# Performance work log

Hardware: AMD Instinct MI355X
Metric: run time of the kernel (lower is better)

## Reference

```python
import jax, jax.numpy as jnp
import numpy as np

N_NODES = 100000
MAX_CHILD = 8
X_SIZE = 128
H_SIZE = 128
N_TYPES = 8
W_SCALE = 0.05  # keep gates out of saturation


def setup_inputs() -> dict:
    key = jax.random.key(0)
    ks = jax.random.split(key, 8)
    return {
        "x": jax.random.normal(ks[0], (N_NODES, X_SIZE), jnp.float32),
        "n_h": jax.random.normal(ks[1], (N_NODES, MAX_CHILD, H_SIZE), jnp.float32),
        "n_c": jax.random.normal(ks[2], (N_NODES, MAX_CHILD, H_SIZE), jnp.float32),
        "type_id": jax.random.randint(ks[3], (N_NODES,), 0, N_TYPES, jnp.int64),
        "W_iou": jax.random.normal(ks[4], (N_TYPES, X_SIZE, 3 * H_SIZE), jnp.float32) * W_SCALE,
        "U_iou": jax.random.normal(ks[5], (N_TYPES, H_SIZE, 3 * H_SIZE), jnp.float32) * W_SCALE,
        "b_iou": jnp.zeros((N_TYPES, 3 * H_SIZE), jnp.float32),
        "U_f": jax.random.normal(ks[6], (N_TYPES, H_SIZE, H_SIZE), jnp.float32) * W_SCALE,
        "b_f": jnp.zeros((N_TYPES, H_SIZE), jnp.float32),
    }


def reference(x, n_h, n_c, type_id, W_iou, U_iou, b_iou, U_f, b_f):
    # x: [N, X], n_h/n_c: [N, K, H] child mailbox, type_id: [N]
    N, K, H = n_h.shape
    T = W_iou.shape[0]
    h_sum = n_h.sum(axis=1)  # child-sum is linear -> aggregate before GEMM [N, H]

    # --- reduce_func: masked per-type child aggregation ---
    iou_aggr = jnp.zeros((N, 3 * H), x.dtype)
    c_aggr = jnp.zeros((N, H), x.dtype)
    for t in range(T):
        m = (type_id == t)[:, None]
        iou_t = h_sum @ U_iou[t]                                   # [N, 3H]
        f = jax.nn.sigmoid(jnp.einsum("nkh,hg->nkg", n_h, U_f[t]) + b_f[t])
        c_t = (f * n_c).sum(axis=1)                                # [N, H]
        iou_aggr = jnp.where(m, iou_t, iou_aggr)
        c_aggr = jnp.where(m, c_t, c_aggr)

    # --- apply_node_func: masked per-type node states ---
    h_out = jnp.zeros((N, H), x.dtype)
    c_out = jnp.zeros((N, H), x.dtype)
    for t in range(T):
        m = (type_id == t)[:, None]
        iou = x @ W_iou[t] + iou_aggr + b_iou[t]                   # [N, 3H]
        i_g, o_g, u_g = jnp.split(iou, 3, axis=1)
        c_t = jax.nn.sigmoid(i_g) * jnp.tanh(u_g) + c_aggr
        h_t = jax.nn.sigmoid(o_g) * jnp.tanh(c_t)
        h_out = jnp.where(m, h_t, h_out)
        c_out = jnp.where(m, c_t, c_out)
    return h_out, c_out
```

## Files before the change

### kernel.cpp

```cpp
#include <hip/hip_runtime.h>
#include <hip/hip_bf16.h>
#include <stdint.h>

typedef __bf16 bf16x8 __attribute__((ext_vector_type(8)));
typedef float  f32x4  __attribute__((ext_vector_type(4)));

#define H    128
#define KCH  8
#define NT   8
#define BM   32

#define WS_TILET  2048
#define WS_IDX    16384
#define WS_UF     458752
#define WS_W      720896

__device__ __forceinline__ float fsigm(float v){ return 1.f/(1.f+__expf(-v)); }
__device__ __forceinline__ float ftanh(float v){
  v = fminf(fmaxf(v,-15.f),15.f);
  float e = __expf(2.f*v);
  return (e-1.f)/(e+1.f);
}

__global__ void k_init(int* ws){ if (threadIdx.x < 40) ws[threadIdx.x] = 0; }

__global__ void k_detect(const int* __restrict__ type_id, int* ws){
  __shared__ int nz;
  if (threadIdx.x == 0) nz = 0;
  __syncthreads();
  int v = type_id[threadIdx.x];
  if ((threadIdx.x & 1) && v != 0) atomicAdd(&nz, 1);
  __syncthreads();
  if (threadIdx.x == 0) ws[25] = (nz == 0) ? 2 : 1;
}

__global__ void k_count(const int* __restrict__ type_id, int* __restrict__ ws, int N){
  __shared__ int h[NT];
  int tid = threadIdx.x;
  if (tid < NT) h[tid] = 0;
  __syncthreads();
  int stride = ws[25];
  int i = blockIdx.x*blockDim.x + tid;
  if (i < N) atomicAdd(&h[type_id[(size_t)i*stride]], 1);
  __syncthreads();
  if (tid < NT) atomicAdd(&ws[tid], h[tid]);
}

__global__ void k_scan(int* m){
  int s = 0;
  for (int t=0;t<NT;++t){
    m[16+t] = s;
    m[8+t]  = s;
    m[26+t] = s + m[t];
    s += ((m[t]+BM-1)/BM)*BM;
  }
  m[24] = s;
}

__global__ void k_scatter(const int* __restrict__ type_id, int* __restrict__ ws, int N){
  __shared__ int h[NT], base[NT];
  int tid = threadIdx.x;
  if (tid < NT) h[tid] = 0;
  __syncthreads();
  int stride = ws[25];
  int i = blockIdx.x*blockDim.x + tid;
  int t = 0, lp = 0;
  if (i < N){ t = type_id[(size_t)i*stride]; lp = atomicAdd(&h[t], 1); }
  __syncthreads();
  if (tid < NT) base[tid] = atomicAdd(&ws[8+tid], h[tid]);
  __syncthreads();
  if (i < N) ws[(WS_IDX/4) + base[t] + lp] = i;
}

__global__ void k_tiletype(int* ws, int ntiles){
  int i = blockIdx.x*256 + threadIdx.x;
  if (i >= ntiles) return;
  const int* op = ws + 16;
  int p = i*BM, t = -1;
  if (p < op[8]){
    for (int s=0;s<NT;++s) if (p >= op[s] && p < op[s+1]) t = s;
  }
  ws[(WS_TILET/4) + i] = t;
}

__global__ void k_prep_uf(const float* __restrict__ U_f, char* __restrict__ ws){
  int gid = blockIdx.x*256 + threadIdx.x;
  if (gid >= NT*128*16) return;
  int sp = gid & 15, c = (gid>>4) & 127, t = gid >> 11;
  int kbase = 8*(sp ^ (c & 7));
  const float* src = U_f + ((size_t)t*H + kbase)*H + c;
  bf16x8 v;
  #pragma unroll
  for (int j=0;j<8;++j) v[j] = (__bf16)src[(size_t)j*H];
  *(bf16x8*)(ws + WS_UF + (size_t)gid*16) = v;
}

__global__ void k_prep_w(const float* __restrict__ W_iou, const float* __restrict__ U_iou,
                         char* __restrict__ ws){
  int gid = blockIdx.x*256 + threadIdx.x;
  if (gid >= NT*384*32) return;
  int sp = gid & 31, col = (gid>>5) % 384, t = gid / (384*32);
  int K0 = sp*8;
  bf16x8 v;
  #pragma unroll
  for (int j=0;j<8;++j){
    int K = K0 + j;
    float f = (K < H) ? W_iou[((size_t)t*H + K)*(3*H) + col]
                      : U_iou[((size_t)t*H + (K-H))*(3*H) + col];
    v[j] = (__bf16)f;
  }
  *(bf16x8*)(ws + WS_W + (size_t)gid*16) = v;
}

__global__ __launch_bounds__(256,4) void k_phaseB(
  const float* __restrict__ n_h, const float* __restrict__ n_c,
  const float* __restrict__ b_f, const char* __restrict__ ws,
  float* __restrict__ out, int N)
{
  __shared__ __align__(16) char lds[40960];
  const int* meta = (const int*)ws;
  int tile = blockIdx.x;
  int t = ((const int*)(ws + WS_TILET))[tile];
  if (t < 0) return;
  int ev = meta[26 + t];
  const int* idx = (const int*)(ws + WS_IDX);

  int tid = threadIdx.x;
  int lane = tid & 63, wave = tid >> 6;
  int rw = wave & 1, cw = wave >> 1;
  int l15 = lane & 15, l4 = lane >> 4;
  int base = tile*BM;

  int mrow = tid >> 3, mcol = (tid & 7) * 16;
  int mpos = base + mrow;
  int mnode = (mpos < ev) ? idx[mpos] : 0;

  int npos = base + rw*16 + l15;
  bool valn = npos < ev;
  int nd = valn ? idx[npos] : 0;
  const float* ncb = n_c + (size_t)nd*(KCH*H);
  int ocb[4]; f32x4 bf4[4];
  #pragma unroll
  for (int st=0; st<4; ++st){
    ocb[st] = cw*64 + st*16 + 4*l4;
    bf4[st] = *(const f32x4*)(b_f + t*H + ocb[st]);
  }

  {
    const char* src = ws + WS_UF + (size_t)t*32768;
    #pragma unroll
    for (int it=0; it<8; ++it){
      bf16x8 v = *(const bf16x8*)(src + it*4096 + tid*16);
      *(bf16x8*)(lds + it*4096 + tid*16) = v;
    }
  }

  const float* nh_base = n_h + (size_t)mnode*(KCH*H) + mcol;

  float hsum[16];
  #pragma unroll
  for (int j=0;j<16;++j) hsum[j] = 0.f;
  f32x4 cacc[4];
  #pragma unroll
  for (int st=0;st<4;++st) cacc[st] = (f32x4){0.f,0.f,0.f,0.f};

  int arow = rw*16 + l15;
  int aswz = (arow & 7) << 4;
  int mswz = (mrow & 7) << 4;

  for (int k=0;k<KCH;++k){
    {
      const float4* p = (const float4*)(nh_base + (size_t)k*H);
      float4 a0=p[0], a1=p[1], a2=p[2], a3=p[3];
      hsum[0]+=a0.x;  hsum[1]+=a0.y;  hsum[2]+=a0.z;  hsum[3]+=a0.w;
      hsum[4]+=a1.x;  hsum[5]+=a1.y;  hsum[6]+=a1.z;  hsum[7]+=a1.w;
      hsum[8]+=a2.x;  hsum[9]+=a2.y;  hsum[10]+=a2.z; hsum[11]+=a2.w;
      hsum[12]+=a3.x; hsum[13]+=a3.y; hsum[14]+=a3.z; hsum[15]+=a3.w;
      bf16x8 w0, w1;
      w0[0]=(__bf16)a0.x; w0[1]=(__bf16)a0.y; w0[2]=(__bf16)a0.z; w0[3]=(__bf16)a0.w;
      w0[4]=(__bf16)a1.x; w0[5]=(__bf16)a1.y; w0[6]=(__bf16)a1.z; w0[7]=(__bf16)a1.w;
      w1[0]=(__bf16)a2.x; w1[1]=(__bf16)a2.y; w1[2]=(__bf16)a2.z; w1[3]=(__bf16)a2.w;
      w1[4]=(__bf16)a3.x; w1[5]=(__bf16)a3.y; w1[6]=(__bf16)a3.z; w1[7]=(__bf16)a3.w;
      *(bf16x8*)(lds + 32768 + mrow*256 + (( mcol*2      ) ^ mswz)) = w0;
      *(bf16x8*)(lds + 32768 + mrow*256 + (( mcol*2 + 16 ) ^ mswz)) = w1;
    }
    __syncthreads();

    f32x4 fa[4];
    #pragma unroll
    for (int st=0;st<4;++st) fa[st] = (f32x4){0.f,0.f,0.f,0.f};
    #pragma unroll
    for (int kk=0; kk<4; ++kk){
      int kb = kk*64 + l4*16;
      bf16x8 bnh = *(const bf16x8*)(lds + 32768 + arow*256 + (kb ^ aswz));
      #pragma unroll
      for (int st=0;st<4;++st){
        int c = cw*64 + st*16 + l15;
        bf16x8 auf = *(const bf16x8*)(lds + c*256 + (kb ^ ((c&7)<<4)));
        fa[st] = __builtin_amdgcn_mfma_f32_16x16x32_bf16(auf, bnh, fa[st], 0,0,0);
      }
    }
    #pragma unroll
    for (int st=0;st<4;++st){
      f32x4 nc = *(const f32x4*)(ncb + k*H + ocb[st]);
      #pragma unroll
      for (int r=0;r<4;++r){
        float fg = fsigm(fa[st][r] + bf4[st][r]);
        cacc[st][r] += fg * nc[r];
      }
    }
    __syncthreads();
  }

  if (mpos < ev){
    float4* dst = (float4*)(out + (size_t)mnode*H + mcol);
    dst[0] = make_float4(hsum[0], hsum[1], hsum[2], hsum[3]);
    dst[1] = make_float4(hsum[4], hsum[5], hsum[6], hsum[7]);
    dst[2] = make_float4(hsum[8], hsum[9], hsum[10],hsum[11]);
    dst[3] = make_float4(hsum[12],hsum[13],hsum[14],hsum[15]);
  }
  float* outc = out + (size_t)N*H;
  if (valn){
    #pragma unroll
    for (int st=0;st<4;++st)
      *(f32x4*)(outc + (size_t)nd*H + ocb[st]) = cacc[st];
  }
}

__global__ __launch_bounds__(256,4) void k_phaseA(
  const float* __restrict__ x, const float* __restrict__ b_iou,
  const char* __restrict__ ws, float* __restrict__ out, int N)
{
  __shared__ __align__(16) char lds[16384];
  const int* meta = (const int*)ws;
  int tile = blockIdx.x;
  int t = ((const int*)(ws + WS_TILET))[tile];
  if (t < 0) return;
  int ev = meta[26 + t];
  const int* idx = (const int*)(ws + WS_IDX);

  int tid = threadIdx.x;
  int lane = tid & 63, wave = tid >> 6;
  int rw = wave & 1, cw = wave >> 1;
  int l15 = lane & 15, l4 = lane >> 4;
  int base = tile*BM;

  int mrow = tid >> 3, mcol = (tid & 7) * 16;
  int mpos = base + mrow;
  int mnode = (mpos < ev) ? idx[mpos] : 0;

  int npos = base + rw*16 + l15;
  bool valn = npos < ev;
  int nd = valn ? idx[npos] : 0;

  int mswz = (mrow & 7) << 4;
  {
    const float4* px = (const float4*)(x   + (size_t)mnode*H + mcol);
    const float4* ph = (const float4*)(out + (size_t)mnode*H + mcol);
    float4 x0=px[0], x1=px[1], x2=px[2], x3=px[3];
    float4 h0=ph[0], h1=ph[1], h2=ph[2], h3=ph[3];
    bf16x8 w0,w1,w2,w3;
    w0[0]=(__bf16)x0.x; w0[1]=(__bf16)x0.y; w0[2]=(__bf16)x0.z; w0[3]=(__bf16)x0.w;
    w0[4]=(__bf16)x1.x; w0[5]=(__bf16)x1.y; w0[6]=(__bf16)x1.z; w0[7]=(__bf16)x1.w;
    w1[0]=(__bf16)x2.x; w1[1]=(__bf16)x2.y; w1[2]=(__bf16)x2.z; w1[3]=(__bf16)x2.w;
    w1[4]=(__bf16)x3.x; w1[5]=(__bf16)x3.y; w1[6]=(__bf16)x3.z; w1[7]=(__bf16)x3.w;
    w2[0]=(__bf16)h0.x; w2[1]=(__bf16)h0.y; w2[2]=(__bf16)h0.z; w2[3]=(__bf16)h0.w;
    w2[4]=(__bf16)h1.x; w2[5]=(__bf16)h1.y; w2[6]=(__bf16)h1.z; w2[7]=(__bf16)h1.w;
    w3[0]=(__bf16)h2.x; w3[1]=(__bf16)h2.y; w3[2]=(__bf16)h2.z; w3[3]=(__bf16)h2.w;
    w3[4]=(__bf16)h3.x; w3[5]=(__bf16)h3.y; w3[6]=(__bf16)h3.z; w3[7]=(__bf16)h3.w;
    int ab = mrow*512;
    *(bf16x8*)(lds + ab + (( mcol*2            ) ^ mswz)) = w0;
    *(bf16x8*)(lds + ab + (( mcol*2 + 16       ) ^ mswz)) = w1;
    *(bf16x8*)(lds + ab + (( 256 + mcol*2      ) ^ mswz)) = w2;
    *(bf16x8*)(lds + ab + (( 256 + mcol*2 + 16 ) ^ mswz)) = w3;
  }
  __syncthreads();

  int arow = rw*16 + l15;
  int aswz = (arow & 7) << 4;
  float* outc = out + (size_t)N*H;
  const char* wbase = ws + WS_W + (size_t)t*(384*256*2);

  #pragma unroll
  for (int st=0; st<4; ++st){
    int ocb = cw*64 + st*16 + 4*l4;
    f32x4 ag[3];
    #pragma unroll
    for (int g=0;g<3;++g) ag[g] = (f32x4){0.f,0.f,0.f,0.f};
    const char* wrow = wbase + (size_t)(cw*64 + st*16 + l15)*512;
    #pragma unroll 1
    for (int kc=0;kc<4;++kc){
      #pragma unroll
      for (int kk2=0;kk2<2;++kk2){
        int kb = kc*128 + kk2*64 + l4*16;
        bf16x8 bact = *(const bf16x8*)(lds + arow*512 + (kb ^ aswz));
        #pragma unroll
        for (int g=0;g<3;++g){
          bf16x8 aW = *(const bf16x8*)(wrow + (size_t)(g*128)*512 + kb);
          ag[g] = __builtin_amdgcn_mfma_f32_16x16x32_bf16(aW, bact, ag[g], 0,0,0);
        }
      }
    }
    if (valn){
      f32x4 bi4 = *(const f32x4*)(b_iou + t*(3*H) +        ocb);
      f32x4 bo4 = *(const f32x4*)(b_iou + t*(3*H) + H   +  ocb);
      f32x4 bu4 = *(const f32x4*)(b_iou + t*(3*H) + 2*H +  ocb);
      f32x4 ca  = *(const f32x4*)(outc + (size_t)nd*H + ocb);
      f32x4 hv4, cv4;
      #pragma unroll
      for (int r=0;r<4;++r){
        float ig = ag[0][r] + bi4[r];
        float og = ag[1][r] + bo4[r];
        float ug = ag[2][r] + bu4[r];
        float cv = fsigm(ig)*ftanh(ug) + ca[r];
        float hv = fsigm(og)*ftanh(cv);
        cv4[r] = cv; hv4[r] = hv;
      }
      *(f32x4*)(out  + (size_t)nd*H + ocb) = hv4;
      *(f32x4*)(outc + (size_t)nd*H + ocb) = cv4;
    }
  }
}

extern "C" void kernel_launch(void* const* d_in, const int* in_sizes, int n_in,
                              void* d_out, int out_size, void* d_ws, size_t ws_size,
                              hipStream_t stream){
  const float* x      = (const float*)d_in[0];
  const float* n_h    = (const float*)d_in[1];
  const float* n_c    = (const float*)d_in[2];
  const int*   typ    = (const int*)d_in[3];
  const float* W_iou  = (const float*)d_in[4];
  const float* U_iou  = (const float*)d_in[5];
  const float* b_iou  = (const float*)d_in[6];
  const float* U_f    = (const float*)d_in[7];
  const float* b_f    = (const float*)d_in[8];
  float* out = (float*)d_out;
  int*   ws  = (int*)d_ws;
  char*  wsc = (char*)d_ws;
  int N = in_sizes[0] / H;
  int nb = (N + 255) / 256;
  int ntiles = (N + NT*(BM-1) + BM-1) / BM;

  hipLaunchKernelGGL(k_init,     dim3(1),   dim3(64),  0, stream, ws);
  hipLaunchKernelGGL(k_detect,   dim3(1),   dim3(256), 0, stream, typ, ws);
  hipLaunchKernelGGL(k_count,    dim3(nb),  dim3(256), 0, stream, typ, ws, N);
  hipLaunchKernelGGL(k_scan,     dim3(1),   dim3(1),   0, stream, ws);
  hipLaunchKernelGGL(k_scatter,  dim3(nb),  dim3(256), 0, stream, typ, ws, N);
  hipLaunchKernelGGL(k_tiletype, dim3((ntiles+255)/256), dim3(256), 0, stream, ws, ntiles);
  hipLaunchKernelGGL(k_prep_uf,  dim3((NT*128*16+255)/256), dim3(256), 0, stream, U_f, wsc);
  hipLaunchKernelGGL(k_prep_w,   dim3((NT*384*32+255)/256), dim3(256), 0, stream, W_iou, U_iou, wsc);
  hipLaunchKernelGGL(k_phaseB,   dim3(ntiles), dim3(256), 0, stream,
                     n_h, n_c, b_f, wsc, out, N);
  hipLaunchKernelGGL(k_phaseA,   dim3(ntiles), dim3(256), 0, stream,
                     x, b_iou, wsc, out, N);
}
```

Baseline: 428.9 us.

## Load child hidden states straight into MFMA operands, dropping LDS staging and barriers

In phase B, each lane now reads its n_h fragment directly from global memory into registers in the layout the MFMA B operand expects. This replaces the earlier cooperative load into an LDS buffer, which needed two __syncthreads per child iteration. The child-sum h is also accumulated from these registers, with each column-wave writing its half of the output, and the LDS footprint shrinks to hold only the U_f tile. In exchange, both column-waves load the same n_h rows, doubling global or L2 read traffic for n_h. The child loop is also no longer unrolled.

```diff
diff --git a/kernel.cpp b/kernel.cpp
--- a/kernel.cpp
+++ b/kernel.cpp
@@ -117,7 +117,7 @@
   const float* __restrict__ b_f, const char* __restrict__ ws,
   float* __restrict__ out, int N)
 {
-  __shared__ __align__(16) char lds[40960];
+  __shared__ __align__(16) char lds[32768];
   const int* meta = (const int*)ws;
   int tile = blockIdx.x;
   int t = ((const int*)(ws + WS_TILET))[tile];
@@ -131,13 +131,10 @@
   int l15 = lane & 15, l4 = lane >> 4;
   int base = tile*BM;
 
-  int mrow = tid >> 3, mcol = (tid & 7) * 16;
-  int mpos = base + mrow;
-  int mnode = (mpos < ev) ? idx[mpos] : 0;
-
   int npos = base + rw*16 + l15;
   bool valn = npos < ev;
   int nd = valn ? idx[npos] : 0;
+  const float* nhb = n_h + (size_t)nd*(KCH*H);
   const float* ncb = n_c + (size_t)nd*(KCH*H);
   int ocb[4]; f32x4 bf4[4];
   #pragma unroll
@@ -154,76 +151,71 @@
       *(bf16x8*)(lds + it*4096 + tid*16) = v;
     }
   }
-
-  const float* nh_base = n_h + (size_t)mnode*(KCH*H) + mcol;
-
-  float hsum[16];
-  #pragma unroll
-  for (int j=0;j<16;++j) hsum[j] = 0.f;
+  __syncthreads();
+
   f32x4 cacc[4];
   #pragma unroll
   for (int st=0;st<4;++st) cacc[st] = (f32x4){0.f,0.f,0.f,0.f};
-
-  int arow = rw*16 + l15;
-  int aswz = (arow & 7) << 4;
-  int mswz = (mrow & 7) << 4;
-
+  f32x4 hsv0 = {0,0,0,0}, hsv1 = {0,0,0,0}, hsv2 = {0,0,0,0}, hsv3 = {0,0,0,0};
+
+  #pragma unroll 1
   for (int k=0;k<KCH;++k){
-    {
-      const float4* p = (const float4*)(nh_base + (size_t)k*H);
-      float4 a0=p[0], a1=p[1], a2=p[2], a3=p[3];
-      hsum[0]+=a0.x;  hsum[1]+=a0.y;  hsum[2]+=a0.z;  hsum[3]+=a0.w;
-      hsum[4]+=a1.x;  hsum[5]+=a1.y;  hsum[6]+=a1.z;  hsum[7]+=a1.w;
-      hsum[8]+=a2.x;  hsum[9]+=a2.y;  hsum[10]+=a2.z; hsum[11]+=a2.w;
-      hsum[12]+=a3.x; hsum[13]+=a3.y; hsum[14]+=a3.z; hsum[15]+=a3.w;
-      bf16x8 w0, w1;
-      w0[0]=(__bf16)a0.x; w0[1]=(__bf16)a0.y; w0[2]=(__bf16)a0.z; w0[3]=(__bf16)a0.w;
-      w0[4]=(__bf16)a1.x; w0[5]=(__bf16)a1.y; w0[6]=(__bf16)a1.z; w0[7]=(__bf16)a1.w;
-      w1[0]=(__bf16)a2.x; w1[1]=(__bf16)a2.y; w1[2]=(__bf16)a2.z; w1[3]=(__bf16)a2.w;
-      w1[4]=(__bf16)a3.x; w1[5]=(__bf16)a3.y; w1[6]=(__bf16)a3.z; w1[7]=(__bf16)a3.w;
-      *(bf16x8*)(lds + 32768 + mrow*256 + (( mcol*2      ) ^ mswz)) = w0;
-      *(bf16x8*)(lds + 32768 + mrow*256 + (( mcol*2 + 16 ) ^ mswz)) = w1;
-    }
-    __syncthreads();
+    const float* rowp = nhb + (size_t)k*H + l4*8;
+    f32x4 L0 = *(const f32x4*)(rowp +  0);
+    f32x4 L1 = *(const f32x4*)(rowp +  4);
+    f32x4 L2 = *(const f32x4*)(rowp + 32);
+    f32x4 L3 = *(const f32x4*)(rowp + 36);
+    f32x4 L4 = *(const f32x4*)(rowp + 64);
+    f32x4 L5 = *(const f32x4*)(rowp + 68);
+    f32x4 L6 = *(const f32x4*)(rowp + 96);
+    f32x4 L7 = *(const f32x4*)(rowp +100);
+
+    if (cw == 0){ hsv0 += L0; hsv1 += L1; hsv2 += L2; hsv3 += L3; }
+    else        { hsv0 += L4; hsv1 += L5; hsv2 += L6; hsv3 += L7; }
+
+    bf16x8 bn0, bn1, bn2, bn3;
+    #pragma unroll
+    for (int j=0;j<4;++j){
+      bn0[j]=(__bf16)L0[j]; bn0[4+j]=(__bf16)L1[j];
+      bn1[j]=(__bf16)L2[j]; bn1[4+j]=(__bf16)L3[j];
+      bn2[j]=(__bf16)L4[j]; bn2[4+j]=(__bf16)L5[j];
+      bn3[j]=(__bf16)L6[j]; bn3[4+j]=(__bf16)L7[j];
+    }
 
     f32x4 fa[4];
     #pragma unroll
     for (int st=0;st<4;++st) fa[st] = (f32x4){0.f,0.f,0.f,0.f};
     #pragma unroll
-    for (int kk=0; kk<4; ++kk){
-      int kb = kk*64 + l4*16;
-      bf16x8 bnh = *(const bf16x8*)(lds + 32768 + arow*256 + (kb ^ aswz));
-      #pragma unroll
-      for (int st=0;st<4;++st){
-        int c = cw*64 + st*16 + l15;
-        bf16x8 auf = *(const bf16x8*)(lds + c*256 + (kb ^ ((c&7)<<4)));
-        fa[st] = __builtin_amdgcn_mfma_f32_16x16x32_bf16(auf, bnh, fa[st], 0,0,0);
-      }
-    }
-    #pragma unroll
     for (int st=0;st<4;++st){
-      f32x4 nc = *(const f32x4*)(ncb + k*H + ocb[st]);
+      int c = cw*64 + st*16 + l15;
+      int cs = (c&7)<<4;
+      const char* crow = lds + c*256;
+      fa[st] = __builtin_amdgcn_mfma_f32_16x16x32_bf16(*(const bf16x8*)(crow + ((  0 + l4*16) ^ cs)), bn0, fa[st], 0,0,0);
+      fa[st] = __builtin_amdgcn_mfma_f32_16x16x32_bf16(*(const bf16x8*)(crow + (( 64 + l4*16) ^ cs)), bn1, fa[st], 0,0,0);
+      fa[st] = __builtin_amdgcn_mfma_f32_16x16x32_bf16(*(const bf16x8*)(crow + ((128 + l4*16) ^ cs)), bn2, fa[st], 0,0,0);
+      fa[st] = __builtin_amdgcn_mfma_f32_16x16x32_bf16(*(const bf16x8*)(crow + ((192 + l4*16) ^ cs)), bn3, fa[st], 0,0,0);
+    }
+    #pragma unroll
+    for (int st=0;st<4;++st){
+      f32x4 nc = *(const f32x4*)(ncb + (size_t)k*H + ocb[st]);
       #pragma unroll
       for (int r=0;r<4;++r){
         float fg = fsigm(fa[st][r] + bf4[st][r]);
         cacc[st][r] += fg * nc[r];
       }
     }
-    __syncthreads();
-  }
-
-  if (mpos < ev){
-    float4* dst = (float4*)(out + (size_t)mnode*H + mcol);
-    dst[0] = make_float4(hsum[0], hsum[1], hsum[2], hsum[3]);
-    dst[1] = make_float4(hsum[4], hsum[5], hsum[6], hsum[7]);
-    dst[2] = make_float4(hsum[8], hsum[9], hsum[10],hsum[11]);
-    dst[3] = make_float4(hsum[12],hsum[13],hsum[14],hsum[15]);
-  }
-  float* outc = out + (size_t)N*H;
+  }
+
   if (valn){
+    float* oh = out + (size_t)nd*H + cw*64 + l4*8;
+    *(f32x4*)(oh     ) = hsv0;
+    *(f32x4*)(oh +  4) = hsv1;
+    *(f32x4*)(oh + 32) = hsv2;
+    *(f32x4*)(oh + 36) = hsv3;
+    float* outc = out + (size_t)N*H + (size_t)nd*H;
     #pragma unroll
     for (int st=0;st<4;++st)
-      *(f32x4*)(outc + (size_t)nd*H + ocb[st]) = cacc[st];
+      *(f32x4*)(outc + ocb[st]) = cacc[st];
   }
 }
 
```

Result: slower. 562.4 us (+31.1%).

## Double-buffer child mailbox tiles in phaseB to overlap loads with MFMA

Applied to the files above, without the earlier changes.

Splits the phaseB child-hidden staging area into two LDS buffers and prefetches the next child's n_h row into registers while the current child's forget-gate MFMAs run. The n_c loads are also hoisted ahead of the MFMA loop, so each child step needs one barrier instead of two. The cost is more LDS and registers, so launch bounds drop from 4 to 3 blocks per CU. The apply kernel's K loop is also unrolled by 2.

```diff
diff --git a/kernel.cpp b/kernel.cpp
--- a/kernel.cpp
+++ b/kernel.cpp
@@ -112,12 +112,12 @@
   *(bf16x8*)(ws + WS_W + (size_t)gid*16) = v;
 }
 
-__global__ __launch_bounds__(256,4) void k_phaseB(
+__global__ __launch_bounds__(256,3) void k_phaseB(
   const float* __restrict__ n_h, const float* __restrict__ n_c,
   const float* __restrict__ b_f, const char* __restrict__ ws,
   float* __restrict__ out, int N)
 {
-  __shared__ __align__(16) char lds[40960];
+  __shared__ __align__(16) char lds[49152];
   const int* meta = (const int*)ws;
   int tile = blockIdx.x;
   int t = ((const int*)(ws + WS_TILET))[tile];
@@ -168,23 +168,35 @@
   int aswz = (arow & 7) << 4;
   int mswz = (mrow & 7) << 4;
 
+  {
+    const float4* p = (const float4*)nh_base;
+    float4 a0=p[0], a1=p[1], a2=p[2], a3=p[3];
+    hsum[0]+=a0.x;  hsum[1]+=a0.y;  hsum[2]+=a0.z;  hsum[3]+=a0.w;
+    hsum[4]+=a1.x;  hsum[5]+=a1.y;  hsum[6]+=a1.z;  hsum[7]+=a1.w;
+    hsum[8]+=a2.x;  hsum[9]+=a2.y;  hsum[10]+=a2.z; hsum[11]+=a2.w;
+    hsum[12]+=a3.x; hsum[13]+=a3.y; hsum[14]+=a3.z; hsum[15]+=a3.w;
+    bf16x8 w0, w1;
+    w0[0]=(__bf16)a0.x; w0[1]=(__bf16)a0.y; w0[2]=(__bf16)a0.z; w0[3]=(__bf16)a0.w;
+    w0[4]=(__bf16)a1.x; w0[5]=(__bf16)a1.y; w0[6]=(__bf16)a1.z; w0[7]=(__bf16)a1.w;
+    w1[0]=(__bf16)a2.x; w1[1]=(__bf16)a2.y; w1[2]=(__bf16)a2.z; w1[3]=(__bf16)a2.w;
+    w1[4]=(__bf16)a3.x; w1[5]=(__bf16)a3.y; w1[6]=(__bf16)a3.z; w1[7]=(__bf16)a3.w;
+    *(bf16x8*)(lds + 32768 + mrow*256 + (( mcol*2      ) ^ mswz)) = w0;
+    *(bf16x8*)(lds + 32768 + mrow*256 + (( mcol*2 + 16 ) ^ mswz)) = w1;
+  }
+  __syncthreads();
+
+  #pragma unroll 1
   for (int k=0;k<KCH;++k){
-    {
-      const float4* p = (const float4*)(nh_base + (size_t)k*H);
-      float4 a0=p[0], a1=p[1], a2=p[2], a3=p[3];
-      hsum[0]+=a0.x;  hsum[1]+=a0.y;  hsum[2]+=a0.z;  hsum[3]+=a0.w;
-      hsum[4]+=a1.x;  hsum[5]+=a1.y;  hsum[6]+=a1.z;  hsum[7]+=a1.w;
-      hsum[8]+=a2.x;  hsum[9]+=a2.y;  hsum[10]+=a2.z; hsum[11]+=a2.w;
-      hsum[12]+=a3.x; hsum[13]+=a3.y; hsum[14]+=a3.z; hsum[15]+=a3.w;
-      bf16x8 w0, w1;
-      w0[0]=(__bf16)a0.x; w0[1]=(__bf16)a0.y; w0[2]=(__bf16)a0.z; w0[3]=(__bf16)a0.w;
-      w0[4]=(__bf16)a1.x; w0[5]=(__bf16)a1.y; w0[6]=(__bf16)a1.z; w0[7]=(__bf16)a1.w;
-      w1[0]=(__bf16)a2.x; w1[1]=(__bf16)a2.y; w1[2]=(__bf16)a2.z; w1[3]=(__bf16)a2.w;
-      w1[4]=(__bf16)a3.x; w1[5]=(__bf16)a3.y; w1[6]=(__bf16)a3.z; w1[7]=(__bf16)a3.w;
-      *(bf16x8*)(lds + 32768 + mrow*256 + (( mcol*2      ) ^ mswz)) = w0;
-      *(bf16x8*)(lds + 32768 + mrow*256 + (( mcol*2 + 16 ) ^ mswz)) = w1;
-    }
-    __syncthreads();
+    const int cur = 32768 + (k&1)*8192;
+    const int nxt = 32768 + ((k+1)&1)*8192;
+    float4 b0,b1,b2,b3;
+    if (k < KCH-1){
+      const float4* p = (const float4*)(nh_base + (size_t)(k+1)*H);
+      b0=p[0]; b1=p[1]; b2=p[2]; b3=p[3];
+    }
+    f32x4 nc4[4];
+    #pragma unroll
+    for (int st=0;st<4;++st) nc4[st] = *(const f32x4*)(ncb + (size_t)k*H + ocb[st]);
 
     f32x4 fa[4];
     #pragma unroll
@@ -192,7 +204,7 @@
     #pragma unroll
     for (int kk=0; kk<4; ++kk){
       int kb = kk*64 + l4*16;
-      bf16x8 bnh = *(const bf16x8*)(lds + 32768 + arow*256 + (kb ^ aswz));
+      bf16x8 bnh = *(const bf16x8*)(lds + cur + arow*256 + (kb ^ aswz));
       #pragma unroll
       for (int st=0;st<4;++st){
         int c = cw*64 + st*16 + l15;
@@ -202,12 +214,25 @@
     }
     #pragma unroll
     for (int st=0;st<4;++st){
-      f32x4 nc = *(const f32x4*)(ncb + k*H + ocb[st]);
       #pragma unroll
       for (int r=0;r<4;++r){
         float fg = fsigm(fa[st][r] + bf4[st][r]);
-        cacc[st][r] += fg * nc[r];
+        cacc[st][r] += fg * nc4[st][r];
       }
+    }
+
+    if (k < KCH-1){
+      hsum[0]+=b0.x;  hsum[1]+=b0.y;  hsum[2]+=b0.z;  hsum[3]+=b0.w;
+      hsum[4]+=b1.x;  hsum[5]+=b1.y;  hsum[6]+=b1.z;  hsum[7]+=b1.w;
+      hsum[8]+=b2.x;  hsum[9]+=b2.y;  hsum[10]+=b2.z; hsum[11]+=b2.w;
+      hsum[12]+=b3.x; hsum[13]+=b3.y; hsum[14]+=b3.z; hsum[15]+=b3.w;
+      bf16x8 w0, w1;
+      w0[0]=(__bf16)b0.x; w0[1]=(__bf16)b0.y; w0[2]=(__bf16)b0.z; w0[3]=(__bf16)b0.w;
+      w0[4]=(__bf16)b1.x; w0[5]=(__bf16)b1.y; w0[6]=(__bf16)b1.z; w0[7]=(__bf16)b1.w;
+      w1[0]=(__bf16)b2.x; w1[1]=(__bf16)b2.y; w1[2]=(__bf16)b2.z; w1[3]=(__bf16)b2.w;
+      w1[4]=(__bf16)b3.x; w1[5]=(__bf16)b3.y; w1[6]=(__bf16)b3.z; w1[7]=(__bf16)b3.w;
+      *(bf16x8*)(lds + nxt + mrow*256 + (( mcol*2      ) ^ mswz)) = w0;
+      *(bf16x8*)(lds + nxt + mrow*256 + (( mcol*2 + 16 ) ^ mswz)) = w1;
     }
     __syncthreads();
   }
@@ -288,7 +313,7 @@
     #pragma unroll
     for (int g=0;g<3;++g) ag[g] = (f32x4){0.f,0.f,0.f,0.f};
     const char* wrow = wbase + (size_t)(cw*64 + st*16 + l15)*512;
-    #pragma unroll 1
+    #pragma unroll 2
     for (int kc=0;kc<4;++kc){
       #pragma unroll
       for (int kk2=0;kk2<2;++kk2){
```

Measured after the change: 416.5 us. 2.9% less time.
